# Optimization experiments

Hardware: AMD Instinct MI355X
Metric: run time of the kernel (lower is better)

The kernel has to match this reference:

```python
import jax, jax.numpy as jnp
import numpy as np

N_NODES = 50000
N_EDGES = 800000
D_IN = 128
D_OUT = 64


def setup_inputs() -> dict:
    key = jax.random.key(0)
    k1, k2, k3, k4 = jax.random.split(key, 4)
    x = jax.random.normal(k1, (N_NODES, D_IN), dtype=jnp.float32)
    W = jax.random.normal(k2, (D_OUT, D_IN), dtype=jnp.float32) * (1.0 / np.sqrt(D_IN))
    b = jnp.zeros((D_OUT,), dtype=jnp.float32)
    row = jax.random.randint(k3, (N_EDGES,), 0, N_NODES, dtype=jnp.int32)
    col = jax.random.randint(k4, (N_EDGES,), 0, N_NODES, dtype=jnp.int32)
    return {"x": x, "W": W, "b": b, "row": row, "col": col}


def reference(x, W, b, row, col):
    # Linear projection: [N, D_in] -> [N, D_out]
    h = x @ W.T + b
    n = x.shape[0]
    # Row-normalized SpMM: out[i] = (1/deg(i)) * sum_{(i,j) in E} h[j]
    msg = h[col]  # gather source features: [E, D_out]
    summed = jax.ops.segment_sum(msg, row, num_segments=n)
    deg = jax.ops.segment_sum(jnp.ones_like(row, dtype=h.dtype), row, num_segments=n)
    out = summed / jnp.maximum(deg, 1.0)[:, None]
    return out
```

## Files before the change

kernel.cpp:

```cpp
#include <hip/hip_runtime.h>
#include <hip/hip_bf16.h>

#define D_IN   128
#define D_OUT  64
#define CAP    64
#define MAX_USHORT_NODES 65536
#define BIN_SHIFT 8
#define MAX_BINS  256
#define BIN_CAP   8192
#define P1_BLOCKS 256
#define FAT_THREADS 512
#define SPLIT 4
#define SPLIT_SHIFT 2

using frag_ab = __attribute__((ext_vector_type(8))) short;
using frag_cd = __attribute__((ext_vector_type(4))) float;

static __device__ __forceinline__ short f2bf(float f) {
    union { float f; unsigned u; } v; v.f = f;
    unsigned r = v.u + 0x7FFFu + ((v.u >> 16) & 1u);
    return (short)(r >> 16);
}
static __device__ __forceinline__ float bflo(unsigned w) {
    union { unsigned u; float f; } v; v.u = w << 16; return v.f;
}
static __device__ __forceinline__ float bfhi(unsigned w) {
    union { unsigned u; float f; } v; v.u = w & 0xFFFF0000u; return v.f;
}

__global__ __launch_bounds__(FAT_THREADS)
void proj_bin1_kernel(const float* __restrict__ x,
                      const float* __restrict__ W,
                      const float* __restrict__ bvec,
                      unsigned short* __restrict__ h,
                      const int* __restrict__ row, const int* __restrict__ col,
                      unsigned* __restrict__ scratch, int* __restrict__ cursor,
                      int* __restrict__ ovfA_cnt, unsigned* __restrict__ ovfA_list,
                      int ovfA_cap, int n_nodes, int n_edges, int n_bins) {
    __shared__ int hist[MAX_BINS];
    __shared__ int base[MAX_BINS];

    if ((int)blockIdx.x < P1_BLOCKS) {
        const int per = (n_edges + P1_BLOCKS - 1) / P1_BLOCKS;
        const int e0 = (int)blockIdx.x * per;
        const int e1 = min(e0 + per, n_edges);

        for (int i = threadIdx.x; i < n_bins; i += FAT_THREADS) hist[i] = 0;
        __syncthreads();
        for (int e = e0 + (int)threadIdx.x; e < e1; e += FAT_THREADS)
            atomicAdd(&hist[row[e] >> BIN_SHIFT], 1);
        __syncthreads();
        for (int i = threadIdx.x; i < n_bins; i += FAT_THREADS) {
            const int hcnt = hist[i];
            base[i] = hcnt > 0 ? atomicAdd(&cursor[i * 16], hcnt) : 0;
            hist[i] = 0;
        }
        __syncthreads();
        for (int e = e0 + (int)threadIdx.x; e < e1; e += FAT_THREADS) {
            const int r = row[e];
            const int c = col[e];
            const int bn = r >> BIN_SHIFT;
            const int loc = atomicAdd(&hist[bn], 1);
            const int off = base[bn] + loc;
            if (off < BIN_CAP) {
                scratch[(size_t)bn * BIN_CAP + off] =
                    (unsigned)(r & 255) | ((unsigned)c << 8);
            } else {
                const int k = atomicAdd(ovfA_cnt, 1);
                if (k < ovfA_cap) ovfA_list[k] = (unsigned)r | ((unsigned)c << 16);
            }
        }
        return;
    }

    const int lane = (int)threadIdx.x & 63;
    const int wid  = (int)(((blockIdx.x - P1_BLOCKS) * blockDim.x + threadIdx.x) >> 6);
    const int nwaves = (int)(((gridDim.x - P1_BLOCKS) * blockDim.x) >> 6);
    const int m    = lane & 15;
    const int quad = lane >> 4;

    frag_ab Bf[4][4];
#pragma unroll
    for (int kk = 0; kk < 4; ++kk) {
#pragma unroll
        for (int nt = 0; nt < 4; ++nt) {
            const float* wp = W + (size_t)(nt * 16 + m) * D_IN + kk * 32 + quad * 8;
            const float4 w0 = *(const float4*)wp;
            const float4 w1 = *(const float4*)(wp + 4);
            frag_ab f;
            f[0] = f2bf(w0.x); f[1] = f2bf(w0.y); f[2] = f2bf(w0.z); f[3] = f2bf(w0.w);
            f[4] = f2bf(w1.x); f[5] = f2bf(w1.y); f[6] = f2bf(w1.z); f[7] = f2bf(w1.w);
            Bf[kk][nt] = f;
        }
    }
    float bb[4];
#pragma unroll
    for (int nt = 0; nt < 4; ++nt) bb[nt] = bvec[nt * 16 + m];

    const int ntiles = (n_nodes + 15) / 16;
    for (int tile = wid; tile < ntiles; tile += nwaves) {
        const int node_base = tile * 16;
        int arow = node_base + m;
        if (arow > n_nodes - 1) arow = n_nodes - 1;

        float4 xv[8];
        const float* xr = x + (size_t)arow * D_IN + quad * 8;
#pragma unroll
        for (int kk = 0; kk < 4; ++kk) {
            xv[2 * kk]     = *(const float4*)(xr + kk * 32);
            xv[2 * kk + 1] = *(const float4*)(xr + kk * 32 + 4);
        }

        frag_cd acc[4];
#pragma unroll
        for (int nt = 0; nt < 4; ++nt) {
            acc[nt][0] = bb[nt]; acc[nt][1] = bb[nt];
            acc[nt][2] = bb[nt]; acc[nt][3] = bb[nt];
        }
#pragma unroll
        for (int kk = 0; kk < 4; ++kk) {
            const float4 x0 = xv[2 * kk], x1 = xv[2 * kk + 1];
            frag_ab A;
            A[0] = f2bf(x0.x); A[1] = f2bf(x0.y); A[2] = f2bf(x0.z); A[3] = f2bf(x0.w);
            A[4] = f2bf(x1.x); A[5] = f2bf(x1.y); A[6] = f2bf(x1.z); A[7] = f2bf(x1.w);
#pragma unroll
            for (int nt = 0; nt < 4; ++nt)
                acc[nt] = __builtin_amdgcn_mfma_f32_16x16x32_bf16(A, Bf[kk][nt],
                                                                  acc[nt], 0, 0, 0);
        }
#pragma unroll
        for (int nt = 0; nt < 4; ++nt) {
#pragma unroll
            for (int r = 0; r < 4; ++r) {
                const int node = node_base + quad * 4 + r;
                if (node < n_nodes)
                    h[(size_t)node * D_OUT + nt * 16 + m] =
                        (unsigned short)f2bf(acc[nt][r]);
            }
        }
    }
}

__global__ __launch_bounds__(FAT_THREADS)
void bin_gather_kernel(const unsigned* __restrict__ scratch,
                       const int* __restrict__ cursor,
                       const uint2* __restrict__ h64,
                       int* __restrict__ deg,
                       const unsigned* __restrict__ ovfA_list,
                       const int* __restrict__ ovfA_cnt, int ovfA_cap,
                       int* __restrict__ ovfB_cnt, unsigned* __restrict__ ovfB_list,
                       int ovfB_cap,
                       float4* __restrict__ out4, int n_nodes) {
    __shared__ int ldeg[64];
    __shared__ unsigned short lbuck[64 * CAP];
    const int bin   = (int)blockIdx.x >> SPLIT_SHIFT;
    const int slice = (int)blockIdx.x & (SPLIT - 1);
    const int node0 = (bin << BIN_SHIFT) + (slice << 6);

    int cnt = cursor[bin * 16]; if (cnt > BIN_CAP) cnt = BIN_CAP;

    if (threadIdx.x < 64) ldeg[threadIdx.x] = 0;
    __syncthreads();

    for (int i = threadIdx.x; i < cnt; i += FAT_THREADS) {
        const unsigned rec = scratch[(size_t)bin * BIN_CAP + i];
        const int rl = (int)(rec & 255u);
        if ((rl >> 6) == slice) {
            const int r6 = rl & 63;
            const int s = atomicAdd(&ldeg[r6], 1);
            if (s < CAP) {
                lbuck[(r6 << 6) + s] = (unsigned short)(rec >> 8);
            } else {
                const int k = atomicAdd(ovfB_cnt, 1);
                if (k < ovfB_cap)
                    ovfB_list[k] = (unsigned)(node0 + r6) | ((rec >> 8) << 16);
            }
        }
    }
    int cA = *ovfA_cnt; if (cA > ovfA_cap) cA = ovfA_cap;
    for (int i = threadIdx.x; i < cA; i += FAT_THREADS) {
        const unsigned rec = ovfA_list[i];
        const int r = (int)(rec & 0xFFFFu);
        if ((r >> 6) == ((bin << 2) | slice)) atomicAdd(&ldeg[r & 63], 1);
    }
    __syncthreads();

    if (threadIdx.x < 64 && node0 + (int)threadIdx.x < n_nodes)
        deg[node0 + threadIdx.x] = ldeg[threadIdx.x];

    const int lane = (int)threadIdx.x & 63;
    const int q = lane >> 4;
    const int j = lane & 15;
    const int w = (int)threadIdx.x >> 6;

    for (int r6 = w; r6 < 64; r6 += 8) {
        const int node = node0 + r6;
        if (node >= n_nodes) continue;
        const int d = ldeg[r6];
        const int dc = d < CAP ? d : CAP;
        const int ngr = (dc + 3) >> 2;
        const unsigned short* brow = &lbuck[r6 << 6];

        float a0 = 0.f, a1 = 0.f, a2 = 0.f, a3 = 0.f;
        float b0 = 0.f, b1 = 0.f, b2 = 0.f, b3 = 0.f;
        int g = 0;
        for (; g + 2 <= ngr; g += 2) {
            const int iA = (int)brow[4 * g + q];
            const int iB = (int)brow[4 * g + 4 + q];
            uint2 wA = h64[(size_t)iA * 16 + j];
            uint2 wB = h64[(size_t)iB * 16 + j];
            if (4 * g + q >= dc)     { wA.x = 0u; wA.y = 0u; }
            if (4 * g + 4 + q >= dc) { wB.x = 0u; wB.y = 0u; }
            a0 += bflo(wA.x); a1 += bfhi(wA.x); a2 += bflo(wA.y); a3 += bfhi(wA.y);
            b0 += bflo(wB.x); b1 += bfhi(wB.x); b2 += bflo(wB.y); b3 += bfhi(wB.y);
        }
        for (; g < ngr; ++g) {
            const int iA = (int)brow[4 * g + q];
            uint2 wA = h64[(size_t)iA * 16 + j];
            if (4 * g + q >= dc) { wA.x = 0u; wA.y = 0u; }
            a0 += bflo(wA.x); a1 += bfhi(wA.x); a2 += bflo(wA.y); a3 += bfhi(wA.y);
        }
        a0 += b0; a1 += b1; a2 += b2; a3 += b3;
        a0 += __shfl_xor(a0, 16); a0 += __shfl_xor(a0, 32);
        a1 += __shfl_xor(a1, 16); a1 += __shfl_xor(a1, 32);
        a2 += __shfl_xor(a2, 16); a2 += __shfl_xor(a2, 32);
        a3 += __shfl_xor(a3, 16); a3 += __shfl_xor(a3, 32);
        if (q == 0) {
            const float inv = 1.0f / fmaxf((float)d, 1.0f);
            float4 o;
            o.x = a0 * inv; o.y = a1 * inv; o.z = a2 * inv; o.w = a3 * inv;
            out4[(size_t)node * (D_OUT / 4) + j] = o;
        }
    }
}

__global__ void ovf_apply_kernel(const unsigned short* __restrict__ h,
                                 const int* __restrict__ deg,
                                 const unsigned* __restrict__ listA,
                                 const int* __restrict__ cntA_p, int capA,
                                 const unsigned* __restrict__ listB,
                                 const int* __restrict__ cntB_p, int capB,
                                 float* __restrict__ out) {
    int cA = *cntA_p; if (cA > capA) cA = capA;
    int cB = *cntB_p; if (cB > capB) cB = capB;
    const long long n_tasks = (long long)(cA + cB) * D_OUT;
    long long t = (long long)blockIdx.x * blockDim.x + threadIdx.x;
    const long long stride = (long long)gridDim.x * blockDim.x;
    for (; t < n_tasks; t += stride) {
        const int k = (int)(t >> 6);
        const int lane = (int)(t & 63);
        const unsigned rec = (k < cA) ? listA[k] : listB[k - cA];
        const int r = (int)(rec & 0xFFFFu);
        const int c = (int)(rec >> 16);
        union { unsigned u; float f; } v;
        v.u = ((unsigned)h[(size_t)c * D_OUT + lane]) << 16;
        atomicAdd(&out[(size_t)r * D_OUT + lane],
                  v.f / fmaxf((float)deg[r], 1.0f));
    }
}

__global__ void proj_only_kernel(const float* __restrict__ x,
                                 const float* __restrict__ W,
                                 const float* __restrict__ bvec,
                                 float* __restrict__ h, int n_nodes) {
    const int lane = (int)threadIdx.x & 63;
    const int wave = (int)((blockIdx.x * blockDim.x + threadIdx.x) >> 6);
    const int nwaves = (int)((gridDim.x * blockDim.x) >> 6);
    const float bias = bvec[lane];
    for (int node = wave; node < n_nodes; node += nwaves) {
        const float* xr = &x[(size_t)node * D_IN];
        float acc = bias;
#pragma unroll
        for (int k = 0; k < D_IN; ++k) acc += xr[k] * W[lane * D_IN + k];
        h[(size_t)node * D_OUT + lane] = acc;
    }
}

__global__ void scatter_kernel(const float* __restrict__ h,
                               const int* __restrict__ row,
                               const int* __restrict__ col,
                               float* __restrict__ out,
                               int* __restrict__ deg,
                               long long n_tasks) {
    long long t = (long long)blockIdx.x * blockDim.x + threadIdx.x;
    const long long stride = (long long)gridDim.x * blockDim.x;
    for (; t < n_tasks; t += stride) {
        const int e = (int)(t >> 6);
        const int c = (int)(t & 63);
        atomicAdd(&out[(size_t)row[e] * D_OUT + c], h[(size_t)col[e] * D_OUT + c]);
        if (c == 0) atomicAdd(&deg[row[e]], 1);
    }
}

__global__ void div_kernel(float* __restrict__ out,
                           const int* __restrict__ deg, int n_total) {
    int t = blockIdx.x * blockDim.x + threadIdx.x;
    if (t < n_total) {
        out[t] *= 1.0f / fmaxf((float)deg[t >> 6], 1.0f);
    }
}

extern "C" void kernel_launch(void* const* d_in, const int* in_sizes, int n_in,
                              void* d_out, int out_size, void* d_ws, size_t ws_size,
                              hipStream_t stream) {
    const float* x   = (const float*)d_in[0];
    const float* W   = (const float*)d_in[1];
    const float* b   = (const float*)d_in[2];
    const int*   row = (const int*)d_in[3];
    const int*   col = (const int*)d_in[4];
    float* out = (float*)d_out;

    const int n_nodes = in_sizes[0] / D_IN;
    const int n_edges = in_sizes[3];
    const int n_bins  = (n_nodes + 255) >> BIN_SHIFT;

    char* p = (char*)d_ws;
    unsigned short* h = (unsigned short*)p;
    p += (size_t)n_nodes * D_OUT * sizeof(unsigned short);
    int* deg = (int*)p;            p += (size_t)n_nodes * sizeof(int);
    int* ovf_cnts = (int*)p;       p += 256;
    int* cursor = (int*)p;         p += (size_t)MAX_BINS * 16 * sizeof(int);
    unsigned* ovfA_list = (unsigned*)p;  p += (size_t)n_edges * sizeof(unsigned);
    unsigned* ovfB_list = (unsigned*)p;  p += (size_t)n_edges * sizeof(unsigned);
    unsigned* scratch = (unsigned*)p;
    p += (size_t)n_bins * BIN_CAP * sizeof(unsigned);
    const size_t needed = (size_t)(p - (char*)d_ws);

    if (ws_size >= needed && n_nodes <= MAX_USHORT_NODES) {
        hipMemsetAsync(ovf_cnts, 0, 256 + (size_t)MAX_BINS * 16 * sizeof(int),
                       stream);

        const int ntiles = (n_nodes + 15) / 16;
        int proj_blocks = (ntiles + 15) / 16;
        if (proj_blocks < 1) proj_blocks = 1;
        proj_bin1_kernel<<<P1_BLOCKS + proj_blocks, FAT_THREADS, 0, stream>>>(
            x, W, b, h, row, col, scratch, cursor, &ovf_cnts[0], ovfA_list,
            n_edges, n_nodes, n_edges, n_bins);

        bin_gather_kernel<<<n_bins * SPLIT, FAT_THREADS, 0, stream>>>(
            scratch, cursor, (const uint2*)h, deg, ovfA_list, &ovf_cnts[0],
            n_edges, &ovf_cnts[1], ovfB_list, n_edges, (float4*)out, n_nodes);

        ovf_apply_kernel<<<256, 256, 0, stream>>>(h, deg, ovfA_list,
                                                  &ovf_cnts[0], n_edges,
                                                  ovfB_list, &ovf_cnts[1],
                                                  n_edges, out);
    } else {
        float* hf = (float*)d_ws;
        int* degf = (int*)((char*)d_ws + (size_t)n_nodes * D_OUT * sizeof(float));
        hipMemsetAsync(out, 0, (size_t)out_size * sizeof(float), stream);
        hipMemsetAsync(degf, 0, (size_t)n_nodes * sizeof(int), stream);
        proj_only_kernel<<<1024, 256, 0, stream>>>(x, W, b, hf, n_nodes);
        const long long n_tasks = (long long)n_edges * D_OUT;
        scatter_kernel<<<16384, 256, 0, stream>>>(hf, row, col, out, degf, n_tasks);
        const int n_total = n_nodes * D_OUT;
        div_kernel<<<(n_total + 255) / 256, 256, 0, stream>>>(out, degf, n_total);
    }
}
```

Before: 126.0 us.

## Shrink edge bins to 64 nodes, drop slice split, use nontemporal loads/stores

Edge bins now cover 64 nodes each (1024 bins with a 4096 capacity) instead of 256 nodes split into four slices. Each gather block therefore reads only its own records rather than scanning a whole bin and discarding three quarters of it. The projection loads of x and the output stores use nontemporal hints to reduce cache pollution. The tradeoffs are four times as many bins, which adds cursor atomics and histogram work in the binning phase. The smaller per-bin capacity also raises the chance that records spill to the overflow list.

```diff
diff --git a/kernel.cpp b/kernel.cpp
--- a/kernel.cpp
+++ b/kernel.cpp
@@ -5,16 +5,15 @@
 #define D_OUT  64
 #define CAP    64
 #define MAX_USHORT_NODES 65536
-#define BIN_SHIFT 8
-#define MAX_BINS  256
-#define BIN_CAP   8192
+#define BIN_SHIFT 6
+#define MAX_BINS  1024
+#define BIN_CAP   4096
 #define P1_BLOCKS 256
 #define FAT_THREADS 512
-#define SPLIT 4
-#define SPLIT_SHIFT 2
 
 using frag_ab = __attribute__((ext_vector_type(8))) short;
 using frag_cd = __attribute__((ext_vector_type(4))) float;
+using vfloat4 = __attribute__((ext_vector_type(4))) float;
 
 static __device__ __forceinline__ short f2bf(float f) {
     union { float f; unsigned u; } v; v.f = f;
@@ -64,7 +63,7 @@
             const int off = base[bn] + loc;
             if (off < BIN_CAP) {
                 scratch[(size_t)bn * BIN_CAP + off] =
-                    (unsigned)(r & 255) | ((unsigned)c << 8);
+                    (unsigned)(r & 63) | ((unsigned)c << 6);
             } else {
                 const int k = atomicAdd(ovfA_cnt, 1);
                 if (k < ovfA_cap) ovfA_list[k] = (unsigned)r | ((unsigned)c << 16);
@@ -103,12 +102,12 @@
         int arow = node_base + m;
         if (arow > n_nodes - 1) arow = n_nodes - 1;
 
-        float4 xv[8];
+        vfloat4 xv[8];
         const float* xr = x + (size_t)arow * D_IN + quad * 8;
 #pragma unroll
         for (int kk = 0; kk < 4; ++kk) {
-            xv[2 * kk]     = *(const float4*)(xr + kk * 32);
-            xv[2 * kk + 1] = *(const float4*)(xr + kk * 32 + 4);
+            xv[2 * kk]     = __builtin_nontemporal_load((const vfloat4*)(xr + kk * 32));
+            xv[2 * kk + 1] = __builtin_nontemporal_load((const vfloat4*)(xr + kk * 32 + 4));
         }
 
         frag_cd acc[4];
@@ -119,7 +118,7 @@
         }
 #pragma unroll
         for (int kk = 0; kk < 4; ++kk) {
-            const float4 x0 = xv[2 * kk], x1 = xv[2 * kk + 1];
+            const vfloat4 x0 = xv[2 * kk], x1 = xv[2 * kk + 1];
             frag_ab A;
             A[0] = f2bf(x0.x); A[1] = f2bf(x0.y); A[2] = f2bf(x0.z); A[3] = f2bf(x0.w);
             A[4] = f2bf(x1.x); A[5] = f2bf(x1.y); A[6] = f2bf(x1.z); A[7] = f2bf(x1.w);
@@ -150,12 +149,11 @@
                        const int* __restrict__ ovfA_cnt, int ovfA_cap,
                        int* __restrict__ ovfB_cnt, unsigned* __restrict__ ovfB_list,
                        int ovfB_cap,
-                       float4* __restrict__ out4, int n_nodes) {
+                       float* __restrict__ out, int n_nodes) {
     __shared__ int ldeg[64];
     __shared__ unsigned short lbuck[64 * CAP];
-    const int bin   = (int)blockIdx.x >> SPLIT_SHIFT;
-    const int slice = (int)blockIdx.x & (SPLIT - 1);
-    const int node0 = (bin << BIN_SHIFT) + (slice << 6);
+    const int bin   = (int)blockIdx.x;
+    const int node0 = bin << BIN_SHIFT;
 
     int cnt = cursor[bin * 16]; if (cnt > BIN_CAP) cnt = BIN_CAP;
 
@@ -164,24 +162,21 @@
 
     for (int i = threadIdx.x; i < cnt; i += FAT_THREADS) {
         const unsigned rec = scratch[(size_t)bin * BIN_CAP + i];
-        const int rl = (int)(rec & 255u);
-        if ((rl >> 6) == slice) {
-            const int r6 = rl & 63;
-            const int s = atomicAdd(&ldeg[r6], 1);
-            if (s < CAP) {
-                lbuck[(r6 << 6) + s] = (unsigned short)(rec >> 8);
-            } else {
-                const int k = atomicAdd(ovfB_cnt, 1);
-                if (k < ovfB_cap)
-                    ovfB_list[k] = (unsigned)(node0 + r6) | ((rec >> 8) << 16);
-            }
+        const int rl = (int)(rec & 63u);
+        const int s = atomicAdd(&ldeg[rl], 1);
+        if (s < CAP) {
+            lbuck[(rl << 6) + s] = (unsigned short)(rec >> 6);
+        } else {
+            const int k = atomicAdd(ovfB_cnt, 1);
+            if (k < ovfB_cap)
+                ovfB_list[k] = (unsigned)(node0 + rl) | ((rec >> 6) << 16);
         }
     }
     int cA = *ovfA_cnt; if (cA > ovfA_cap) cA = ovfA_cap;
     for (int i = threadIdx.x; i < cA; i += FAT_THREADS) {
         const unsigned rec = ovfA_list[i];
         const int r = (int)(rec & 0xFFFFu);
-        if ((r >> 6) == ((bin << 2) | slice)) atomicAdd(&ldeg[r & 63], 1);
+        if ((r >> BIN_SHIFT) == bin) atomicAdd(&ldeg[r & 63], 1);
     }
     __syncthreads();
 
@@ -227,9 +222,10 @@
         a3 += __shfl_xor(a3, 16); a3 += __shfl_xor(a3, 32);
         if (q == 0) {
             const float inv = 1.0f / fmaxf((float)d, 1.0f);
-            float4 o;
+            vfloat4 o;
             o.x = a0 * inv; o.y = a1 * inv; o.z = a2 * inv; o.w = a3 * inv;
-            out4[(size_t)node * (D_OUT / 4) + j] = o;
+            __builtin_nontemporal_store(
+                o, (vfloat4*)(out + (size_t)node * D_OUT + j * 4));
         }
     }
 }
@@ -312,7 +308,7 @@
 
     const int n_nodes = in_sizes[0] / D_IN;
     const int n_edges = in_sizes[3];
-    const int n_bins  = (n_nodes + 255) >> BIN_SHIFT;
+    const int n_bins  = (n_nodes + 63) >> BIN_SHIFT;
 
     char* p = (char*)d_ws;
     unsigned short* h = (unsigned short*)p;
@@ -327,7 +323,7 @@
     const size_t needed = (size_t)(p - (char*)d_ws);
 
     if (ws_size >= needed && n_nodes <= MAX_USHORT_NODES) {
-        hipMemsetAsync(ovf_cnts, 0, 256 + (size_t)MAX_BINS * 16 * sizeof(int),
+        hipMemsetAsync(ovf_cnts, 0, 256 + (size_t)n_bins * 16 * sizeof(int),
                        stream);
 
         const int ntiles = (n_nodes + 15) / 16;
@@ -337,9 +333,9 @@
             x, W, b, h, row, col, scratch, cursor, &ovf_cnts[0], ovfA_list,
             n_edges, n_nodes, n_edges, n_bins);
 
-        bin_gather_kernel<<<n_bins * SPLIT, FAT_THREADS, 0, stream>>>(
+        bin_gather_kernel<<<n_bins, FAT_THREADS, 0, stream>>>(
             scratch, cursor, (const uint2*)h, deg, ovfA_list, &ovf_cnts[0],
-            n_edges, &ovf_cnts[1], ovfB_list, n_edges, (float4*)out, n_nodes);
+            n_edges, &ovf_cnts[1], ovfB_list, n_edges, out, n_nodes);
 
         ovf_apply_kernel<<<256, 256, 0, stream>>>(h, deg, ovfA_list,
                                                   &ovf_cnts[0], n_edges,
```

New measurement: 134.5 us. +6.8%, slower.

## Replace global bin cursors with per-block fixed segments, drop memset and counting pass

Applied to the files above, without the earlier changes.

The binning pass no longer runs a histogram pass plus global atomic cursor reservation per bin. Each producer block now writes edges into its own fixed-capacity segment per bin, and per-block counts are stored in a table. Because nothing relies on zeroed global counters, the memset launch goes away. Overflow lists become per-block and per-gather-block instead of using global atomics. In exchange, the gather kernel must scan 256 segments per bin, with one wave per segment and many partly empty or out-of-slice reads, and the workspace footprint grows.

```diff
diff --git a/kernel.cpp b/kernel.cpp
--- a/kernel.cpp
+++ b/kernel.cpp
@@ -7,11 +7,11 @@
 #define MAX_USHORT_NODES 65536
 #define BIN_SHIFT 8
 #define MAX_BINS  256
-#define BIN_CAP   8192
+#define SEG_CAP   64
+#define OVFB_CAP  16384
 #define P1_BLOCKS 256
+#define SPLIT 4
 #define FAT_THREADS 512
-#define SPLIT 4
-#define SPLIT_SHIFT 2
 
 using frag_ab = __attribute__((ext_vector_type(8))) short;
 using frag_cd = __attribute__((ext_vector_type(4))) float;
@@ -34,48 +34,47 @@
                       const float* __restrict__ bvec,
                       unsigned short* __restrict__ h,
                       const int* __restrict__ row, const int* __restrict__ col,
-                      unsigned* __restrict__ scratch, int* __restrict__ cursor,
-                      int* __restrict__ ovfA_cnt, unsigned* __restrict__ ovfA_list,
-                      int ovfA_cap, int n_nodes, int n_edges, int n_bins) {
+                      unsigned* __restrict__ scratch, int* __restrict__ counts,
+                      int* __restrict__ ovfA_cnts, unsigned* __restrict__ ovfA_list,
+                      int per_blkA, int n_nodes, int n_edges, int n_bins) {
     __shared__ int hist[MAX_BINS];
-    __shared__ int base[MAX_BINS];
+    __shared__ int lovf;
 
     if ((int)blockIdx.x < P1_BLOCKS) {
+        const int blk = (int)blockIdx.x;
         const int per = (n_edges + P1_BLOCKS - 1) / P1_BLOCKS;
-        const int e0 = (int)blockIdx.x * per;
+        const int e0 = blk * per;
         const int e1 = min(e0 + per, n_edges);
 
         for (int i = threadIdx.x; i < n_bins; i += FAT_THREADS) hist[i] = 0;
-        __syncthreads();
-        for (int e = e0 + (int)threadIdx.x; e < e1; e += FAT_THREADS)
-            atomicAdd(&hist[row[e] >> BIN_SHIFT], 1);
-        __syncthreads();
-        for (int i = threadIdx.x; i < n_bins; i += FAT_THREADS) {
-            const int hcnt = hist[i];
-            base[i] = hcnt > 0 ? atomicAdd(&cursor[i * 16], hcnt) : 0;
-            hist[i] = 0;
-        }
+        if (threadIdx.x == 0) lovf = 0;
         __syncthreads();
         for (int e = e0 + (int)threadIdx.x; e < e1; e += FAT_THREADS) {
             const int r = row[e];
             const int c = col[e];
             const int bn = r >> BIN_SHIFT;
             const int loc = atomicAdd(&hist[bn], 1);
-            const int off = base[bn] + loc;
-            if (off < BIN_CAP) {
-                scratch[(size_t)bn * BIN_CAP + off] =
+            if (loc < SEG_CAP) {
+                scratch[((size_t)bn * P1_BLOCKS + blk) * SEG_CAP + loc] =
                     (unsigned)(r & 255) | ((unsigned)c << 8);
             } else {
-                const int k = atomicAdd(ovfA_cnt, 1);
-                if (k < ovfA_cap) ovfA_list[k] = (unsigned)r | ((unsigned)c << 16);
+                const int k = atomicAdd(&lovf, 1);
+                if (k < per_blkA)
+                    ovfA_list[(size_t)blk * per_blkA + k] =
+                        (unsigned)r | ((unsigned)c << 16);
             }
         }
+        __syncthreads();
+        for (int i = threadIdx.x; i < n_bins; i += FAT_THREADS)
+            counts[i * P1_BLOCKS + blk] = min(hist[i], SEG_CAP);
+        if (threadIdx.x == 0) ovfA_cnts[blk] = min(lovf, per_blkA);
         return;
     }
 
     const int lane = (int)threadIdx.x & 63;
-    const int wid  = (int)(((blockIdx.x - P1_BLOCKS) * blockDim.x + threadIdx.x) >> 6);
-    const int nwaves = (int)(((gridDim.x - P1_BLOCKS) * blockDim.x) >> 6);
+    const int wid  = ((int)blockIdx.x - P1_BLOCKS) * (FAT_THREADS >> 6)
+                   + ((int)threadIdx.x >> 6);
+    const int nwaves = ((int)gridDim.x - P1_BLOCKS) * (FAT_THREADS >> 6);
     const int m    = lane & 15;
     const int quad = lane >> 4;
 
@@ -143,56 +142,74 @@
 
 __global__ __launch_bounds__(FAT_THREADS)
 void bin_gather_kernel(const unsigned* __restrict__ scratch,
-                       const int* __restrict__ cursor,
+                       const int* __restrict__ counts,
                        const uint2* __restrict__ h64,
                        int* __restrict__ deg,
                        const unsigned* __restrict__ ovfA_list,
-                       const int* __restrict__ ovfA_cnt, int ovfA_cap,
-                       int* __restrict__ ovfB_cnt, unsigned* __restrict__ ovfB_list,
-                       int ovfB_cap,
-                       float4* __restrict__ out4, int n_nodes) {
+                       const int* __restrict__ ovfA_cnts, int per_blkA,
+                       int* __restrict__ ovfB_cnts, unsigned* __restrict__ ovfB_list,
+                       float* __restrict__ out, int n_nodes) {
     __shared__ int ldeg[64];
     __shared__ unsigned short lbuck[64 * CAP];
-    const int bin   = (int)blockIdx.x >> SPLIT_SHIFT;
-    const int slice = (int)blockIdx.x & (SPLIT - 1);
+    __shared__ int scnt[P1_BLOCKS];
+    __shared__ int lovfB;
+    __shared__ int anyA;
+
+    const int g     = (int)blockIdx.x;
+    const int bin   = g >> 2;
+    const int slice = g & (SPLIT - 1);
     const int node0 = (bin << BIN_SHIFT) + (slice << 6);
-
-    int cnt = cursor[bin * 16]; if (cnt > BIN_CAP) cnt = BIN_CAP;
-
-    if (threadIdx.x < 64) ldeg[threadIdx.x] = 0;
+    const int gslice = node0 >> 6;
+    const int tid = (int)threadIdx.x;
+    const int lane = tid & 63;
+    const int w = tid >> 6;
+
+    if (tid < 64) ldeg[tid] = 0;
+    if (tid == 0) { lovfB = 0; anyA = 0; }
     __syncthreads();
 
-    for (int i = threadIdx.x; i < cnt; i += FAT_THREADS) {
-        const unsigned rec = scratch[(size_t)bin * BIN_CAP + i];
-        const int rl = (int)(rec & 255u);
-        if ((rl >> 6) == slice) {
-            const int r6 = rl & 63;
-            const int s = atomicAdd(&ldeg[r6], 1);
-            if (s < CAP) {
-                lbuck[(r6 << 6) + s] = (unsigned short)(rec >> 8);
-            } else {
-                const int k = atomicAdd(ovfB_cnt, 1);
-                if (k < ovfB_cap)
-                    ovfB_list[k] = (unsigned)(node0 + r6) | ((rec >> 8) << 16);
+    for (int i = tid; i < P1_BLOCKS; i += FAT_THREADS)
+        scnt[i] = counts[bin * P1_BLOCKS + i];
+    if (tid < P1_BLOCKS && ovfA_cnts[tid] > 0) anyA = 1;
+    __syncthreads();
+
+    for (int seg = w; seg < P1_BLOCKS; seg += 8) {
+        const int cnt = scnt[seg];
+        if (lane < cnt) {
+            const unsigned rec =
+                scratch[((size_t)bin * P1_BLOCKS + seg) * SEG_CAP + lane];
+            const int rl = (int)(rec & 255u);
+            if ((rl >> 6) == slice) {
+                const int r6 = rl & 63;
+                const int s = atomicAdd(&ldeg[r6], 1);
+                if (s < CAP) {
+                    lbuck[(r6 << 6) + s] = (unsigned short)(rec >> 8);
+                } else {
+                    const int k = atomicAdd(&lovfB, 1);
+                    if (k < OVFB_CAP)
+                        ovfB_list[(size_t)g * OVFB_CAP + k] =
+                            (unsigned)(node0 + r6) | ((rec >> 8) << 16);
+                }
             }
         }
     }
-    int cA = *ovfA_cnt; if (cA > ovfA_cap) cA = ovfA_cap;
-    for (int i = threadIdx.x; i < cA; i += FAT_THREADS) {
-        const unsigned rec = ovfA_list[i];
-        const int r = (int)(rec & 0xFFFFu);
-        if ((r >> 6) == ((bin << 2) | slice)) atomicAdd(&ldeg[r & 63], 1);
+    if (anyA) {
+        for (int blk = 0; blk < P1_BLOCKS; ++blk) {
+            int cA = ovfA_cnts[blk]; if (cA > per_blkA) cA = per_blkA;
+            for (int i = tid; i < cA; i += FAT_THREADS) {
+                const unsigned rec = ovfA_list[(size_t)blk * per_blkA + i];
+                const int r = (int)(rec & 0xFFFFu);
+                if ((r >> 6) == gslice) atomicAdd(&ldeg[r & 63], 1);
+            }
+        }
     }
     __syncthreads();
 
-    if (threadIdx.x < 64 && node0 + (int)threadIdx.x < n_nodes)
-        deg[node0 + threadIdx.x] = ldeg[threadIdx.x];
-
-    const int lane = (int)threadIdx.x & 63;
+    if (tid == 0) ovfB_cnts[g] = min(lovfB, OVFB_CAP);
+    if (tid < 64 && node0 + tid < n_nodes) deg[node0 + tid] = ldeg[tid];
+
     const int q = lane >> 4;
     const int j = lane & 15;
-    const int w = (int)threadIdx.x >> 6;
-
     for (int r6 = w; r6 < 64; r6 += 8) {
         const int node = node0 + r6;
         if (node >= n_nodes) continue;
@@ -203,21 +220,21 @@
 
         float a0 = 0.f, a1 = 0.f, a2 = 0.f, a3 = 0.f;
         float b0 = 0.f, b1 = 0.f, b2 = 0.f, b3 = 0.f;
-        int g = 0;
-        for (; g + 2 <= ngr; g += 2) {
-            const int iA = (int)brow[4 * g + q];
-            const int iB = (int)brow[4 * g + 4 + q];
+        int g2 = 0;
+        for (; g2 + 2 <= ngr; g2 += 2) {
+            const int iA = (int)brow[4 * g2 + q];
+            const int iB = (int)brow[4 * g2 + 4 + q];
             uint2 wA = h64[(size_t)iA * 16 + j];
             uint2 wB = h64[(size_t)iB * 16 + j];
-            if (4 * g + q >= dc)     { wA.x = 0u; wA.y = 0u; }
-            if (4 * g + 4 + q >= dc) { wB.x = 0u; wB.y = 0u; }
+            if (4 * g2 + q >= dc)     { wA.x = 0u; wA.y = 0u; }
+            if (4 * g2 + 4 + q >= dc) { wB.x = 0u; wB.y = 0u; }
             a0 += bflo(wA.x); a1 += bfhi(wA.x); a2 += bflo(wA.y); a3 += bfhi(wA.y);
             b0 += bflo(wB.x); b1 += bfhi(wB.x); b2 += bflo(wB.y); b3 += bfhi(wB.y);
         }
-        for (; g < ngr; ++g) {
-            const int iA = (int)brow[4 * g + q];
+        for (; g2 < ngr; ++g2) {
+            const int iA = (int)brow[4 * g2 + q];
             uint2 wA = h64[(size_t)iA * 16 + j];
-            if (4 * g + q >= dc) { wA.x = 0u; wA.y = 0u; }
+            if (4 * g2 + q >= dc) { wA.x = 0u; wA.y = 0u; }
             a0 += bflo(wA.x); a1 += bfhi(wA.x); a2 += bflo(wA.y); a3 += bfhi(wA.y);
         }
         a0 += b0; a1 += b1; a2 += b2; a3 += b3;
@@ -229,33 +246,39 @@
             const float inv = 1.0f / fmaxf((float)d, 1.0f);
             float4 o;
             o.x = a0 * inv; o.y = a1 * inv; o.z = a2 * inv; o.w = a3 * inv;
-            out4[(size_t)node * (D_OUT / 4) + j] = o;
+            *(float4*)(out + (size_t)node * D_OUT + j * 4) = o;
         }
     }
 }
 
 __global__ void ovf_apply_kernel(const unsigned short* __restrict__ h,
                                  const int* __restrict__ deg,
-                                 const unsigned* __restrict__ listA,
-                                 const int* __restrict__ cntA_p, int capA,
-                                 const unsigned* __restrict__ listB,
-                                 const int* __restrict__ cntB_p, int capB,
+                                 const unsigned* __restrict__ ovfA_list,
+                                 const int* __restrict__ ovfA_cnts, int per_blkA,
+                                 int nA,
+                                 const unsigned* __restrict__ ovfB_list,
+                                 const int* __restrict__ ovfB_cnts, int nB,
                                  float* __restrict__ out) {
-    int cA = *cntA_p; if (cA > capA) cA = capA;
-    int cB = *cntB_p; if (cB > capB) cB = capB;
-    const long long n_tasks = (long long)(cA + cB) * D_OUT;
-    long long t = (long long)blockIdx.x * blockDim.x + threadIdx.x;
-    const long long stride = (long long)gridDim.x * blockDim.x;
-    for (; t < n_tasks; t += stride) {
-        const int k = (int)(t >> 6);
-        const int lane = (int)(t & 63);
-        const unsigned rec = (k < cA) ? listA[k] : listB[k - cA];
-        const int r = (int)(rec & 0xFFFFu);
-        const int c = (int)(rec >> 16);
-        union { unsigned u; float f; } v;
-        v.u = ((unsigned)h[(size_t)c * D_OUT + lane]) << 16;
-        atomicAdd(&out[(size_t)r * D_OUT + lane],
-                  v.f / fmaxf((float)deg[r], 1.0f));
+    for (int lst = (int)blockIdx.x; lst < nA + nB; lst += (int)gridDim.x) {
+        const bool isA = lst < nA;
+        int cnt = isA ? ovfA_cnts[lst] : ovfB_cnts[lst - nA];
+        const int cap = isA ? per_blkA : OVFB_CAP;
+        if (cnt > cap) cnt = cap;
+        if (cnt <= 0) continue;
+        const unsigned* list = isA ? ovfA_list + (size_t)lst * per_blkA
+                                   : ovfB_list + (size_t)(lst - nA) * OVFB_CAP;
+        const long long n_tasks = (long long)cnt * D_OUT;
+        for (long long t = threadIdx.x; t < n_tasks; t += blockDim.x) {
+            const int k = (int)(t >> 6);
+            const int ln = (int)(t & 63);
+            const unsigned rec = list[k];
+            const int r = (int)(rec & 0xFFFFu);
+            const int c = (int)(rec >> 16);
+            union { unsigned u; float f; } v;
+            v.u = ((unsigned)h[(size_t)c * D_OUT + ln]) << 16;
+            atomicAdd(&out[(size_t)r * D_OUT + ln],
+                      v.f / fmaxf((float)deg[r], 1.0f));
+        }
     }
 }
 
@@ -313,38 +336,40 @@
     const int n_nodes = in_sizes[0] / D_IN;
     const int n_edges = in_sizes[3];
     const int n_bins  = (n_nodes + 255) >> BIN_SHIFT;
+    const int n_gb    = n_bins * SPLIT;
+    const int per_blkA = (n_edges + P1_BLOCKS - 1) / P1_BLOCKS;
 
     char* p = (char*)d_ws;
     unsigned short* h = (unsigned short*)p;
     p += (size_t)n_nodes * D_OUT * sizeof(unsigned short);
-    int* deg = (int*)p;            p += (size_t)n_nodes * sizeof(int);
-    int* ovf_cnts = (int*)p;       p += 256;
-    int* cursor = (int*)p;         p += (size_t)MAX_BINS * 16 * sizeof(int);
-    unsigned* ovfA_list = (unsigned*)p;  p += (size_t)n_edges * sizeof(unsigned);
-    unsigned* ovfB_list = (unsigned*)p;  p += (size_t)n_edges * sizeof(unsigned);
+    int* deg = (int*)p;         p += (size_t)n_nodes * sizeof(int);
+    int* ovfA_cnts = (int*)p;   p += (size_t)P1_BLOCKS * sizeof(int);
+    int* ovfB_cnts = (int*)p;   p += (size_t)n_gb * sizeof(int);
+    int* counts = (int*)p;      p += (size_t)n_bins * P1_BLOCKS * sizeof(int);
+    unsigned* ovfA_list = (unsigned*)p;
+    p += (size_t)P1_BLOCKS * per_blkA * sizeof(unsigned);
+    unsigned* ovfB_list = (unsigned*)p;
+    p += (size_t)n_gb * OVFB_CAP * sizeof(unsigned);
     unsigned* scratch = (unsigned*)p;
-    p += (size_t)n_bins * BIN_CAP * sizeof(unsigned);
+    p += (size_t)n_bins * P1_BLOCKS * SEG_CAP * sizeof(unsigned);
     const size_t needed = (size_t)(p - (char*)d_ws);
 
     if (ws_size >= needed && n_nodes <= MAX_USHORT_NODES) {
-        hipMemsetAsync(ovf_cnts, 0, 256 + (size_t)MAX_BINS * 16 * sizeof(int),
-                       stream);
-
         const int ntiles = (n_nodes + 15) / 16;
         int proj_blocks = (ntiles + 15) / 16;
         if (proj_blocks < 1) proj_blocks = 1;
         proj_bin1_kernel<<<P1_BLOCKS + proj_blocks, FAT_THREADS, 0, stream>>>(
-            x, W, b, h, row, col, scratch, cursor, &ovf_cnts[0], ovfA_list,
-            n_edges, n_nodes, n_edges, n_bins);
-
-        bin_gather_kernel<<<n_bins * SPLIT, FAT_THREADS, 0, stream>>>(
-            scratch, cursor, (const uint2*)h, deg, ovfA_list, &ovf_cnts[0],
-            n_edges, &ovf_cnts[1], ovfB_list, n_edges, (float4*)out, n_nodes);
-
-        ovf_apply_kernel<<<256, 256, 0, stream>>>(h, deg, ovfA_list,
-                                                  &ovf_cnts[0], n_edges,
-                                                  ovfB_list, &ovf_cnts[1],
-                                                  n_edges, out);
+            x, W, b, h, row, col, scratch, counts, ovfA_cnts, ovfA_list,
+            per_blkA, n_nodes, n_edges, n_bins);
+
+        bin_gather_kernel<<<n_gb, FAT_THREADS, 0, stream>>>(
+            scratch, counts, (const uint2*)h, deg, ovfA_list, ovfA_cnts,
+            per_blkA, ovfB_cnts, ovfB_list, out, n_nodes);
+
+        ovf_apply_kernel<<<256, 256, 0, stream>>>(h, deg, ovfA_list, ovfA_cnts,
+                                                  per_blkA, P1_BLOCKS,
+                                                  ovfB_list, ovfB_cnts, n_gb,
+                                                  out);
     } else {
         float* hf = (float*)d_ws;
         int* degf = (int*)((char*)d_ws + (size_t)n_nodes * D_OUT * sizeof(float));
```

After: 132.3 us. +5.0%, slower.

## Fold overflow edges into gather kernel via shared accumulators and drop apply kernel

Applied to the files above, without the earlier changes.

Overflow edges are now handled inside the gather kernel. Per-node overflow beyond CAP is accumulated into a shared-memory float buffer, and bin-overflow edges are folded back into the local buckets. This removes the separate ovf_apply kernel launch and its global atomics. The main gather loop is also unrolled to four groups to expose more memory-level parallelism. The cost is 16KB of extra LDS per block plus a zeroing pass, which may reduce occupancy, and shared-memory atomics on the rare overflow path.

```diff
diff --git a/kernel.cpp b/kernel.cpp
--- a/kernel.cpp
+++ b/kernel.cpp
@@ -26,6 +26,20 @@
 }
 static __device__ __forceinline__ float bfhi(unsigned w) {
     union { unsigned u; float f; } v; v.u = w & 0xFFFF0000u; return v.f;
+}
+
+static __device__ __forceinline__ void facc_accum(float* facc,
+                                                  const uint2* __restrict__ h64,
+                                                  int r6, int c) {
+    const uint2* hr = h64 + (size_t)c * 16;
+#pragma unroll 4
+    for (int t = 0; t < 16; ++t) {
+        const uint2 wv = hr[t];
+        atomicAdd(&facc[(r6 << 6) + t * 4 + 0], bflo(wv.x));
+        atomicAdd(&facc[(r6 << 6) + t * 4 + 1], bfhi(wv.x));
+        atomicAdd(&facc[(r6 << 6) + t * 4 + 2], bflo(wv.y));
+        atomicAdd(&facc[(r6 << 6) + t * 4 + 3], bfhi(wv.y));
+    }
 }
 
 __global__ __launch_bounds__(FAT_THREADS)
@@ -74,8 +88,9 @@
     }
 
     const int lane = (int)threadIdx.x & 63;
-    const int wid  = (int)(((blockIdx.x - P1_BLOCKS) * blockDim.x + threadIdx.x) >> 6);
-    const int nwaves = (int)(((gridDim.x - P1_BLOCKS) * blockDim.x) >> 6);
+    const int wid  = ((int)blockIdx.x - P1_BLOCKS) * (FAT_THREADS >> 6)
+                   + ((int)threadIdx.x >> 6);
+    const int nwaves = ((int)gridDim.x - P1_BLOCKS) * (FAT_THREADS >> 6);
     const int m    = lane & 15;
     const int quad = lane >> 4;
 
@@ -148,50 +163,55 @@
                        int* __restrict__ deg,
                        const unsigned* __restrict__ ovfA_list,
                        const int* __restrict__ ovfA_cnt, int ovfA_cap,
-                       int* __restrict__ ovfB_cnt, unsigned* __restrict__ ovfB_list,
-                       int ovfB_cap,
-                       float4* __restrict__ out4, int n_nodes) {
+                       float* __restrict__ out, int n_nodes) {
     __shared__ int ldeg[64];
     __shared__ unsigned short lbuck[64 * CAP];
-    const int bin   = (int)blockIdx.x >> SPLIT_SHIFT;
-    const int slice = (int)blockIdx.x & (SPLIT - 1);
+    __shared__ float facc[64 * D_OUT];
+    const int g     = (int)blockIdx.x;
+    const int bin   = g >> SPLIT_SHIFT;
+    const int slice = g & (SPLIT - 1);
     const int node0 = (bin << BIN_SHIFT) + (slice << 6);
+    const int tid   = (int)threadIdx.x;
 
     int cnt = cursor[bin * 16]; if (cnt > BIN_CAP) cnt = BIN_CAP;
 
-    if (threadIdx.x < 64) ldeg[threadIdx.x] = 0;
+    if (tid < 64) ldeg[tid] = 0;
+    for (int i = tid; i < 64 * D_OUT; i += FAT_THREADS) facc[i] = 0.f;
     __syncthreads();
 
-    for (int i = threadIdx.x; i < cnt; i += FAT_THREADS) {
+    for (int i = tid; i < cnt; i += FAT_THREADS) {
         const unsigned rec = scratch[(size_t)bin * BIN_CAP + i];
         const int rl = (int)(rec & 255u);
         if ((rl >> 6) == slice) {
             const int r6 = rl & 63;
             const int s = atomicAdd(&ldeg[r6], 1);
-            if (s < CAP) {
-                lbuck[(r6 << 6) + s] = (unsigned short)(rec >> 8);
-            } else {
-                const int k = atomicAdd(ovfB_cnt, 1);
-                if (k < ovfB_cap)
-                    ovfB_list[k] = (unsigned)(node0 + r6) | ((rec >> 8) << 16);
+            if (s < CAP) lbuck[(r6 << 6) + s] = (unsigned short)(rec >> 8);
+            else         facc_accum(facc, h64, r6, (int)(rec >> 8));
+        }
+    }
+    int cA = *ovfA_cnt; if (cA > ovfA_cap) cA = ovfA_cap;
+    if (cA > 0) {
+        const int gslice = node0 >> 6;
+        for (int i = tid; i < cA; i += FAT_THREADS) {
+            const unsigned rec = ovfA_list[i];
+            const int r = (int)(rec & 0xFFFFu);
+            if ((r >> 6) == gslice) {
+                const int r6 = r & 63;
+                const int c = (int)(rec >> 16);
+                const int s = atomicAdd(&ldeg[r6], 1);
+                if (s < CAP) lbuck[(r6 << 6) + s] = (unsigned short)c;
+                else         facc_accum(facc, h64, r6, c);
             }
         }
     }
-    int cA = *ovfA_cnt; if (cA > ovfA_cap) cA = ovfA_cap;
-    for (int i = threadIdx.x; i < cA; i += FAT_THREADS) {
-        const unsigned rec = ovfA_list[i];
-        const int r = (int)(rec & 0xFFFFu);
-        if ((r >> 6) == ((bin << 2) | slice)) atomicAdd(&ldeg[r & 63], 1);
-    }
     __syncthreads();
 
-    if (threadIdx.x < 64 && node0 + (int)threadIdx.x < n_nodes)
-        deg[node0 + threadIdx.x] = ldeg[threadIdx.x];
-
-    const int lane = (int)threadIdx.x & 63;
+    if (tid < 64 && node0 + tid < n_nodes) deg[node0 + tid] = ldeg[tid];
+
+    const int lane = tid & 63;
     const int q = lane >> 4;
     const int j = lane & 15;
-    const int w = (int)threadIdx.x >> 6;
+    const int w = tid >> 6;
 
     for (int r6 = w; r6 < 64; r6 += 8) {
         const int node = node0 + r6;
@@ -203,21 +223,36 @@
 
         float a0 = 0.f, a1 = 0.f, a2 = 0.f, a3 = 0.f;
         float b0 = 0.f, b1 = 0.f, b2 = 0.f, b3 = 0.f;
-        int g = 0;
-        for (; g + 2 <= ngr; g += 2) {
-            const int iA = (int)brow[4 * g + q];
-            const int iB = (int)brow[4 * g + 4 + q];
+        int g2 = 0;
+        for (; g2 + 4 <= ngr; g2 += 4) {
+            const int i0 = (int)brow[4 * g2 + q];
+            const int i1 = (int)brow[4 * g2 + 4 + q];
+            const int i2 = (int)brow[4 * g2 + 8 + q];
+            const int i3 = (int)brow[4 * g2 + 12 + q];
+            uint2 w0 = h64[(size_t)i0 * 16 + j];
+            uint2 w1 = h64[(size_t)i1 * 16 + j];
+            uint2 w2 = h64[(size_t)i2 * 16 + j];
+            uint2 w3 = h64[(size_t)i3 * 16 + j];
+            if (4 * g2 + 12 + q >= dc) { w3.x = 0u; w3.y = 0u; }
+            a0 += bflo(w0.x); a1 += bfhi(w0.x); a2 += bflo(w0.y); a3 += bfhi(w0.y);
+            b0 += bflo(w1.x); b1 += bfhi(w1.x); b2 += bflo(w1.y); b3 += bfhi(w1.y);
+            a0 += bflo(w2.x); a1 += bfhi(w2.x); a2 += bflo(w2.y); a3 += bfhi(w2.y);
+            b0 += bflo(w3.x); b1 += bfhi(w3.x); b2 += bflo(w3.y); b3 += bfhi(w3.y);
+        }
+        for (; g2 + 2 <= ngr; g2 += 2) {
+            const int iA = (int)brow[4 * g2 + q];
+            const int iB = (int)brow[4 * g2 + 4 + q];
             uint2 wA = h64[(size_t)iA * 16 + j];
             uint2 wB = h64[(size_t)iB * 16 + j];
-            if (4 * g + q >= dc)     { wA.x = 0u; wA.y = 0u; }
-            if (4 * g + 4 + q >= dc) { wB.x = 0u; wB.y = 0u; }
+            if (4 * g2 + q >= dc)     { wA.x = 0u; wA.y = 0u; }
+            if (4 * g2 + 4 + q >= dc) { wB.x = 0u; wB.y = 0u; }
             a0 += bflo(wA.x); a1 += bfhi(wA.x); a2 += bflo(wA.y); a3 += bfhi(wA.y);
             b0 += bflo(wB.x); b1 += bfhi(wB.x); b2 += bflo(wB.y); b3 += bfhi(wB.y);
         }
-        for (; g < ngr; ++g) {
-            const int iA = (int)brow[4 * g + q];
+        for (; g2 < ngr; ++g2) {
+            const int iA = (int)brow[4 * g2 + q];
             uint2 wA = h64[(size_t)iA * 16 + j];
-            if (4 * g + q >= dc) { wA.x = 0u; wA.y = 0u; }
+            if (4 * g2 + q >= dc) { wA.x = 0u; wA.y = 0u; }
             a0 += bflo(wA.x); a1 += bfhi(wA.x); a2 += bflo(wA.y); a3 += bfhi(wA.y);
         }
         a0 += b0; a1 += b1; a2 += b2; a3 += b3;
@@ -226,36 +261,13 @@
         a2 += __shfl_xor(a2, 16); a2 += __shfl_xor(a2, 32);
         a3 += __shfl_xor(a3, 16); a3 += __shfl_xor(a3, 32);
         if (q == 0) {
+            const float* fa = &facc[(r6 << 6) + j * 4];
             const float inv = 1.0f / fmaxf((float)d, 1.0f);
             float4 o;
-            o.x = a0 * inv; o.y = a1 * inv; o.z = a2 * inv; o.w = a3 * inv;
-            out4[(size_t)node * (D_OUT / 4) + j] = o;
-        }
-    }
-}
-
-__global__ void ovf_apply_kernel(const unsigned short* __restrict__ h,
-                                 const int* __restrict__ deg,
-                                 const unsigned* __restrict__ listA,
-                                 const int* __restrict__ cntA_p, int capA,
-                                 const unsigned* __restrict__ listB,
-                                 const int* __restrict__ cntB_p, int capB,
-                                 float* __restrict__ out) {
-    int cA = *cntA_p; if (cA > capA) cA = capA;
-    int cB = *cntB_p; if (cB > capB) cB = capB;
-    const long long n_tasks = (long long)(cA + cB) * D_OUT;
-    long long t = (long long)blockIdx.x * blockDim.x + threadIdx.x;
-    const long long stride = (long long)gridDim.x * blockDim.x;
-    for (; t < n_tasks; t += stride) {
-        const int k = (int)(t >> 6);
-        const int lane = (int)(t & 63);
-        const unsigned rec = (k < cA) ? listA[k] : listB[k - cA];
-        const int r = (int)(rec & 0xFFFFu);
-        const int c = (int)(rec >> 16);
-        union { unsigned u; float f; } v;
-        v.u = ((unsigned)h[(size_t)c * D_OUT + lane]) << 16;
-        atomicAdd(&out[(size_t)r * D_OUT + lane],
-                  v.f / fmaxf((float)deg[r], 1.0f));
+            o.x = (a0 + fa[0]) * inv; o.y = (a1 + fa[1]) * inv;
+            o.z = (a2 + fa[2]) * inv; o.w = (a3 + fa[3]) * inv;
+            *(float4*)(out + (size_t)node * D_OUT + j * 4) = o;
+        }
     }
 }
 
@@ -321,7 +333,6 @@
     int* ovf_cnts = (int*)p;       p += 256;
     int* cursor = (int*)p;         p += (size_t)MAX_BINS * 16 * sizeof(int);
     unsigned* ovfA_list = (unsigned*)p;  p += (size_t)n_edges * sizeof(unsigned);
-    unsigned* ovfB_list = (unsigned*)p;  p += (size_t)n_edges * sizeof(unsigned);
     unsigned* scratch = (unsigned*)p;
     p += (size_t)n_bins * BIN_CAP * sizeof(unsigned);
     const size_t needed = (size_t)(p - (char*)d_ws);
@@ -339,12 +350,7 @@
 
         bin_gather_kernel<<<n_bins * SPLIT, FAT_THREADS, 0, stream>>>(
             scratch, cursor, (const uint2*)h, deg, ovfA_list, &ovf_cnts[0],
-            n_edges, &ovf_cnts[1], ovfB_list, n_edges, (float4*)out, n_nodes);
-
-        ovf_apply_kernel<<<256, 256, 0, stream>>>(h, deg, ovfA_list,
-                                                  &ovf_cnts[0], n_edges,
-                                                  ovfB_list, &ovf_cnts[1],
-                                                  n_edges, out);
+            n_edges, out, n_nodes);
     } else {
         float* hf = (float*)d_ws;
         int* degf = (int*)((char*)d_ws + (size_t)n_nodes * D_OUT * sizeof(float));
```

Result: faster. 122.4 us, median of 2 (-2.9%).
